# Performance work log

Measured on AMD Instinct MI355X. Metric: run time of the kernel, lower is better.

## Reference

```python
import jax, jax.numpy as jnp
import numpy as np
from jax import lax

FX, FY = 518.857, 519.469   # NYU-v2 depth intrinsics (cx/cy unused by forward)
B, H, W = 8, 479, 639       # TRAIN_CROP_SIZE = [W, H]; H+1, W+1 divisible by 4
P = 8                       # even PATCH_SIZE -> box-filter output is [H+1, W+1]
EPS = 1e-6


def _coords():
    # u_u0 = x - W/2, v_v0 = y - H/2, broadcast over [B,1,H,W]
    u = jnp.arange(W, dtype=jnp.float32)[None, None, None, :] - W / 2.0
    v = jnp.arange(H, dtype=jnp.float32)[None, None, :, None] - H / 2.0
    return u, v


def _surface_normal(xyz):
    # xyz: [H, W, 3] -> normals [H, W, 3]
    x, y, z = xyz[..., 0], xyz[..., 1], xyz[..., 2]
    # 9 box-filtered moments in a single depthwise conv (the original does 9 conv2d calls)
    mom = jnp.stack([x * x, x * y, x * z, y * y, y * z, z * z, x, y, z], 0)[None]  # [1,9,H,W]
    kern = jnp.ones((9, 1, P, P), xyz.dtype)
    s = lax.conv_general_dilated(mom, kern, (1, 1), [(P // 2, P // 2)] * 2,
                                 feature_group_count=9)[0]  # [9, H+1, W+1]
    xx, xy, xz, yy, yz, zz, xs, ys, zs = s
    ATA = jnp.stack([xx, xy, xz, xy, yy, yz, xz, yz, zz], -1)  # [H+1, W+1, 9]
    Hp, Wp = ATA.shape[0], ATA.shape[1]
    ATA = ATA.reshape(Hp, Wp, 3, 3) + EPS * jnp.eye(3, dtype=xyz.dtype)
    AT1 = jnp.stack([xs, ys, zs], -1)[..., None]  # [H+1, W+1, 3, 1]
    # original loops over 4x4 sub-patches with overlap=0 -> equivalent full-grid solve
    n = jnp.linalg.solve(ATA, AT1)                # [H+1, W+1, 3, 1]
    n = n / jnp.sqrt(jnp.sum(n * n, axis=2, keepdims=True))
    n = n[:-1, :-1, :, 0]                         # [H, W, 3]
    # orient toward camera: flip where dot(n, xyz) > 0
    flip = jnp.sum(n * xyz, axis=2, keepdims=True) > 0
    return jnp.where(flip, -n, n)


def _fit_normals(depth):
    # depth: [B,1,H,W] -> surface normals [B,3,H,W], zeroed where depth <= 0
    u, v = _coords()
    x = u * depth / FX
    y = v * depth / FY
    xyz = jnp.concatenate([x, y, depth], 1).transpose(0, 2, 3, 1)  # [B,H,W,3]
    sn = jax.vmap(_surface_normal)(xyz).transpose(0, 3, 1, 2)      # [B,3,H,W]
    return jnp.where(depth > 0, sn, 0.0)


def setup_inputs() -> dict:
    key = jax.random.key(0)
    k1, k2 = jax.random.split(key)
    prediction = jax.random.uniform(k1, (B, 1, H, W), jnp.float32)
    gt = jax.random.uniform(k2, (B, 1, H, W), jnp.float32)
    return {"prediction": prediction, "gt": gt}


def reference(prediction, gt):
    return jnp.mean(jnp.abs(_fit_normals(prediction) - _fit_normals(gt)))
```

## Files before the change

### kernel.cpp

```cpp
#include <hip/hip_runtime.h>

#define HH 479
#define WW 639
#define BATCH 8
#define NBLK (20 * 60 * 8)


__device__ __forceinline__ void solve_normal(
    float xx, float xy, float xz, float yy, float yz, float zz,
    float xs, float ys, float zs,
    float a_c, float b_c, float d0,
    float* nx, float* ny, float* nz)
{
    const float EPSV = 1e-6f;
    const float inv64 = 1.0f / 64.0f;
    float hx = xs * inv64, hy = ys * inv64, hz = zs * inv64;
    float cxx = fmaf(-hx, xs, xx) + EPSV;
    float cxy = fmaf(-hx, ys, xy);
    float cxz = fmaf(-hx, zs, xz);
    float cyy = fmaf(-hy, ys, yy) + EPSV;
    float cyz = fmaf(-hy, zs, yz);
    float czz = fmaf(-hz, zs, zz) + EPSV;
    float c00 = fmaf(cyy, czz, -cyz * cyz);
    float c01 = fmaf(cxz, cyz, -cxy * czz);
    float c02 = fmaf(cxy, cyz, -cxz * cyy);
    float c11 = fmaf(cxx, czz, -cxz * cxz);
    float c12 = fmaf(cxy, cxz, -cxx * cyz);
    float c22 = fmaf(cxx, cyy, -cxy * cxy);
    float m0 = fmaf(c00, xs, fmaf(c01, ys, c02 * zs));
    float m1 = fmaf(c01, xs, fmaf(c11, ys, c12 * zs));
    float m2 = fmaf(c02, xs, fmaf(c12, ys, c22 * zs));
    float g  = fmaf(m0, a_c, fmaf(m1, b_c, m2));
    float inv = rsqrtf(fmaf(m0, m0, fmaf(m1, m1, m2 * m2)));
    if (g > 0.0f) inv = -inv;
    if (!(d0 > 0.0f)) inv = 0.0f;
    *nx = m0 * inv; *ny = m1 * inv; *nz = m2 * inv;
}

__global__ __launch_bounds__(128, 7)
void ppal_main(const float* __restrict__ pred, const float* __restrict__ gt,
               double* __restrict__ acc)
{
    const int tx = threadIdx.x;
    const int ty = threadIdx.y;
    const int tid = ty * 16 + tx;
    const int j0 = blockIdx.x * 32;
    const int i0 = blockIdx.y * 8;
    const int b  = blockIdx.z;

    const float invFX = 1.0f / 518.857f;
    const float invFY = 1.0f / 519.469f;

    __shared__ float sd[2][15 * 41];
    __shared__ float4 cs4[312];
    __shared__ float  csTb[312];
    __shared__ float  wsum[2];

    const float* src0 = pred + (size_t)b * (HH * WW);
    const float* src1 = gt   + (size_t)b * (HH * WW);
    for (int idx = tid; idx < 15 * 41; idx += 128) {
        int lr = idx / 41, lc = idx - lr * 41;
        int r = i0 - 4 + lr, c = j0 - 4 + lc;
        bool ok = (lc < 39) && (r >= 0) && (r < HH) && (c >= 0) && (c < WW);
        int off = r * WW + c;
        sd[0][idx] = ok ? src0[off] : 0.0f;
        sd[1][idx] = ok ? src1[off] : 0.0f;
    }

    float aw[9];
#pragma unroll
    for (int m = 0; m < 9; ++m)
        aw[m] = ((float)(j0 + 2 * tx + m - 4) - 319.5f) * invFX;
    const float bc = ((float)(i0 + ty) - 239.5f) * invFY;
    const int ebase = ty * 39 + 2 * tx;

    float n0A[3], n1A[3];
    float contrib = 0.0f;

    __syncthreads();

#pragma unroll
    for (int k = 0; k < 2; ++k) {
        if (tid < 78) {
            int g = tid / 39;
            int c = tid - 39 * g;
            int rb = 4 * g;
            const float* col = &sd[k][c];
            float bv = ((float)(i0 + rb - 4) - 239.5f) * invFY;
            float S1 = 0.f, Sb = 0.f, Sbb = 0.f, T1 = 0.f, Tb = 0.f;
#pragma unroll
            for (int r = 0; r < 8; ++r) {
                float d  = col[(rb + r) * 41];
                float bvr = fmaf((float)r, invFY, bv);
                float bd = bvr * d;
                T1 += d;  Tb += bd;
                S1  = fmaf(d,  d,  S1);
                Sb  = fmaf(bd, d,  Sb);
                Sbb = fmaf(bd, bd, Sbb);
            }
            int e = rb * 39 + c;
            cs4[e]  = make_float4(S1, Sb, Sbb, T1);
            csTb[e] = Tb;
#pragma unroll
            for (int s = 1; s < 4; ++s) {
                float d0 = col[(rb + s - 1) * 41];
                float d1 = col[(rb + s + 7) * 41];
                float b0 = fmaf((float)(s - 1), invFY, bv);
                float b1 = fmaf((float)(s + 7), invFY, bv);
                float bd0 = b0 * d0, bd1 = b1 * d1;
                T1 += d1 - d0;
                Tb += bd1 - bd0;
                S1  += fmaf(d1,  d1,  -d0  * d0);
                Sb  += fmaf(bd1, d1,  -bd0 * d0);
                Sbb += fmaf(bd1, bd1, -bd0 * bd0);
                e += 39;
                cs4[e]  = make_float4(S1, Sb, Sbb, T1);
                csTb[e] = Tb;
            }
        }
        __syncthreads();

        {
            float Sxx = 0.f, Sxy = 0.f, Sxz = 0.f, Syy = 0.f, Syz = 0.f;
            float Szz = 0.f, Sxs = 0.f, Sys = 0.f, Szs = 0.f;
#pragma unroll
            for (int m = 1; m < 8; ++m) {
                int e = ebase + m;
                float4 r = cs4[e];
                float  tb = csTb[e];
                Szz += r.x;  Syz += r.y;  Syy += r.z;
                Szs += r.w;  Sys += tb;
                Sxz = fmaf(aw[m],         r.x, Sxz);
                Sxy = fmaf(aw[m],         r.y, Sxy);
                Sxs = fmaf(aw[m],         r.w, Sxs);
                Sxx = fmaf(aw[m] * aw[m], r.x, Sxx);
            }

            float nn[2][3];
#pragma unroll
            for (int p = 0; p < 2; ++p) {
                int m = (p == 0) ? 0 : 8;
                int e = ebase + m;
                float4 r = cs4[e];
                float  tb = csTb[e];
                float xx = fmaf(aw[m] * aw[m], r.x, Sxx);
                float xy = fmaf(aw[m], r.y, Sxy);
                float xz = fmaf(aw[m], r.x, Sxz);
                float yy = Syy + r.z;
                float yz = Syz + r.y;
                float zz = Szz + r.x;
                float xs = fmaf(aw[m], r.w, Sxs);
                float ys = Sys + tb;
                float zs = Szs + r.w;
                float d0 = sd[k][(ty + 4) * 41 + (2 * tx + p + 4)];
                solve_normal(xx, xy, xz, yy, yz, zz, xs, ys, zs,
                             aw[4 + p], bc, d0, &nn[p][0], &nn[p][1], &nn[p][2]);
            }
            if (k == 0) {
                n0A[0] = nn[0][0]; n0A[1] = nn[0][1]; n0A[2] = nn[0][2];
                n1A[0] = nn[1][0]; n1A[1] = nn[1][1]; n1A[2] = nn[1][2];
                __syncthreads();
            } else {
                const int i = i0 + ty;
                const bool valid0 = (i < HH);
                const bool valid1 = (i < HH) && (j0 + 2 * tx + 1 < WW);
                float c0 = fabsf(n0A[0] - nn[0][0]) + fabsf(n0A[1] - nn[0][1])
                         + fabsf(n0A[2] - nn[0][2]);
                float c1 = fabsf(n1A[0] - nn[1][0]) + fabsf(n1A[1] - nn[1][1])
                         + fabsf(n1A[2] - nn[1][2]);
                contrib = (valid0 ? c0 : 0.0f) + (valid1 ? c1 : 0.0f);
            }
        }
    }

    float v = contrib;
#pragma unroll
    for (int off = 32; off > 0; off >>= 1) v += __shfl_down(v, off, 64);
    int wid = tid >> 6, lane = tid & 63;
    if (lane == 0) wsum[wid] = v;
    __syncthreads();
    if (tid == 0) {
        double bs = (double)wsum[0] + (double)wsum[1];
        int slot = blockIdx.x + 20 * blockIdx.y + 1200 * blockIdx.z;
        acc[slot] = bs;
    }
}

__global__ void ppal_finalize(const double* __restrict__ acc, float* __restrict__ out)
{
    int tid = threadIdx.x;
    double v = 0.0;
    for (int s = tid; s < NBLK; s += 256) v += acc[s];
#pragma unroll
    for (int off = 32; off > 0; off >>= 1) v += __shfl_down(v, off, 64);
    __shared__ double wsum[4];
    int wid = tid >> 6, lane = tid & 63;
    if (lane == 0) wsum[wid] = v;
    __syncthreads();
    if (tid == 0)
        out[0] = (float)((wsum[0] + wsum[1] + wsum[2] + wsum[3])
                         * (1.0 / 7345944.0));
}

extern "C" void kernel_launch(void* const* d_in, const int* in_sizes, int n_in,
                              void* d_out, int out_size, void* d_ws, size_t ws_size,
                              hipStream_t stream)
{
    const float* pred = (const float*)d_in[0];
    const float* gt   = (const float*)d_in[1];
    float* out  = (float*)d_out;
    double* acc = (double*)d_ws;

    dim3 grid(20, 60, BATCH);
    dim3 block(16, 8);
    ppal_main<<<grid, block, 0, stream>>>(pred, gt, acc);
    ppal_finalize<<<1, 256, 0, stream>>>(acc, out);
}
```

Before: 101.7 us.

## Replace shared-memory box filter with per-wavefront sliding window and lane-permute sums

```diff
diff --git a/kernel.cpp b/kernel.cpp
--- a/kernel.cpp
+++ b/kernel.cpp
@@ -3,8 +3,19 @@
 #define HH 479
 #define WW 639
 #define BATCH 8
-#define NBLK (20 * 60 * 8)
-
+#define CT 12
+#define RB 30
+#define NBLK (CT * RB * BATCH)
+
+
+__device__ __forceinline__ float box8(float x, int a1, int a2, int a4)
+{
+    float t = x + __int_as_float(
+        __builtin_amdgcn_ds_bpermute(a1, __float_as_int(x)));
+    t += __int_as_float(__builtin_amdgcn_ds_bpermute(a2, __float_as_int(t)));
+    t += __int_as_float(__builtin_amdgcn_ds_bpermute(a4, __float_as_int(t)));
+    return t;
+}
 
 __device__ __forceinline__ void solve_normal(
     float xx, float xy, float xz, float yy, float yz, float zz,
@@ -37,152 +48,134 @@
     *nx = m0 * inv; *ny = m1 * inv; *nz = m2 * inv;
 }
 
-__global__ __launch_bounds__(128, 7)
+__global__ __launch_bounds__(64, 4)
 void ppal_main(const float* __restrict__ pred, const float* __restrict__ gt,
                double* __restrict__ acc)
 {
-    const int tx = threadIdx.x;
-    const int ty = threadIdx.y;
-    const int tid = ty * 16 + tx;
-    const int j0 = blockIdx.x * 32;
-    const int i0 = blockIdx.y * 8;
+    const int lane = threadIdx.x;
+    const int j0 = blockIdx.x * 56;
+    const int r0 = blockIdx.y * 16;
     const int b  = blockIdx.z;
 
     const float invFX = 1.0f / 518.857f;
     const float invFY = 1.0f / 519.469f;
 
-    __shared__ float sd[2][15 * 41];
-    __shared__ float4 cs4[312];
-    __shared__ float  csTb[312];
-    __shared__ float  wsum[2];
-
-    const float* src0 = pred + (size_t)b * (HH * WW);
-    const float* src1 = gt   + (size_t)b * (HH * WW);
-    for (int idx = tid; idx < 15 * 41; idx += 128) {
-        int lr = idx / 41, lc = idx - lr * 41;
-        int r = i0 - 4 + lr, c = j0 - 4 + lc;
-        bool ok = (lc < 39) && (r >= 0) && (r < HH) && (c >= 0) && (c < WW);
-        int off = r * WW + c;
-        sd[0][idx] = ok ? src0[off] : 0.0f;
-        sd[1][idx] = ok ? src1[off] : 0.0f;
+    const float* __restrict__ pA = pred + (size_t)b * (HH * WW);
+    const float* __restrict__ pB = gt   + (size_t)b * (HH * WW);
+
+    const int c = j0 - 4 + lane;
+    const int j = j0 + lane;
+    const bool col_ok = (c >= 0) && (c < WW);
+    const bool pix_ok = (lane < 56) && (j < WW);
+    const float a  = ((float)c - 319.5f) * invFX;
+    const float a2 = a * a;
+    const float ap = ((float)j - 319.5f) * invFX;
+    const int ba1 = ((lane + 1) & 63) << 2;
+    const int ba2 = ((lane + 2) & 63) << 2;
+    const int ba4 = ((lane + 4) & 63) << 2;
+
+    float S1A = 0.f, SbA = 0.f, SbbA = 0.f, T1A = 0.f, TbA = 0.f;
+    float S1B = 0.f, SbB = 0.f, SbbB = 0.f, T1B = 0.f, TbB = 0.f;
+
+    int off = (r0 - 4) * WW + c;
+#pragma unroll
+    for (int w = 0; w < 8; ++w) {
+        int r = r0 - 4 + w;
+        bool ok = col_ok && (r >= 0);
+        int o = ok ? off : 0;
+        float dA = pA[o]; dA = ok ? dA : 0.f;
+        float dB = pB[o]; dB = ok ? dB : 0.f;
+        float bv = ((float)r - 239.5f) * invFY;
+        float bdA = bv * dA, bdB = bv * dB;
+        T1A += dA;  TbA += bdA;
+        S1A = fmaf(dA,  dA,  S1A);
+        SbA = fmaf(bdA, dA,  SbA);
+        SbbA = fmaf(bdA, bdA, SbbA);
+        T1B += dB;  TbB += bdB;
+        S1B = fmaf(dB,  dB,  S1B);
+        SbB = fmaf(bdB, dB,  SbB);
+        SbbB = fmaf(bdB, bdB, SbbB);
+        off += WW;
     }
 
-    float aw[9];
-#pragma unroll
-    for (int m = 0; m < 9; ++m)
-        aw[m] = ((float)(j0 + 2 * tx + m - 4) - 319.5f) * invFX;
-    const float bc = ((float)(i0 + ty) - 239.5f) * invFY;
-    const int ebase = ty * 39 + 2 * tx;
-
-    float n0A[3], n1A[3];
-    float contrib = 0.0f;
-
-    __syncthreads();
-
-#pragma unroll
-    for (int k = 0; k < 2; ++k) {
-        if (tid < 78) {
-            int g = tid / 39;
-            int c = tid - 39 * g;
-            int rb = 4 * g;
-            const float* col = &sd[k][c];
-            float bv = ((float)(i0 + rb - 4) - 239.5f) * invFY;
-            float S1 = 0.f, Sb = 0.f, Sbb = 0.f, T1 = 0.f, Tb = 0.f;
-#pragma unroll
-            for (int r = 0; r < 8; ++r) {
-                float d  = col[(rb + r) * 41];
-                float bvr = fmaf((float)r, invFY, bv);
-                float bd = bvr * d;
-                T1 += d;  Tb += bd;
-                S1  = fmaf(d,  d,  S1);
-                Sb  = fmaf(bd, d,  Sb);
-                Sbb = fmaf(bd, bd, Sbb);
-            }
-            int e = rb * 39 + c;
-            cs4[e]  = make_float4(S1, Sb, Sbb, T1);
-            csTb[e] = Tb;
-#pragma unroll
-            for (int s = 1; s < 4; ++s) {
-                float d0 = col[(rb + s - 1) * 41];
-                float d1 = col[(rb + s + 7) * 41];
-                float b0 = fmaf((float)(s - 1), invFY, bv);
-                float b1 = fmaf((float)(s + 7), invFY, bv);
-                float bd0 = b0 * d0, bd1 = b1 * d1;
-                T1 += d1 - d0;
-                Tb += bd1 - bd0;
-                S1  += fmaf(d1,  d1,  -d0  * d0);
-                Sb  += fmaf(bd1, d1,  -bd0 * d0);
-                Sbb += fmaf(bd1, bd1, -bd0 * bd0);
-                e += 39;
-                cs4[e]  = make_float4(S1, Sb, Sbb, T1);
-                csTb[e] = Tb;
-            }
+    float contrib = 0.f;
+    int off_new = (r0 + 4) * WW + c;
+    int off_old = (r0 - 4) * WW + c;
+    int off_ctr = r0 * WW + j;
+
+    for (int s = 0; s < 16; ++s) {
+        const int i = r0 + s;
+        const bool row_ok = (i < HH);
+
+        {
+            const bool okc = row_ok && pix_ok;
+            int o = okc ? off_ctr : 0;
+            float d0A = pA[o]; d0A = okc ? d0A : 0.f;
+            float d0B = pB[o]; d0B = okc ? d0B : 0.f;
+            float bc = ((float)i - 239.5f) * invFY;
+
+            float hS1  = box8(S1A,      ba1, ba2, ba4);
+            float hSb  = box8(SbA,      ba1, ba2, ba4);
+            float hSbb = box8(SbbA,     ba1, ba2, ba4);
+            float hT1  = box8(T1A,      ba1, ba2, ba4);
+            float hTb  = box8(TbA,      ba1, ba2, ba4);
+            float haS1 = box8(a * S1A,  ba1, ba2, ba4);
+            float haSb = box8(a * SbA,  ba1, ba2, ba4);
+            float haT1 = box8(a * T1A,  ba1, ba2, ba4);
+            float ha2S1= box8(a2 * S1A, ba1, ba2, ba4);
+            float nA[3];
+            solve_normal(ha2S1, haSb, haS1, hSbb, hSb, hS1, haT1, hTb, hT1,
+                         ap, bc, d0A, &nA[0], &nA[1], &nA[2]);
+
+            float gS1  = box8(S1B,      ba1, ba2, ba4);
+            float gSb  = box8(SbB,      ba1, ba2, ba4);
+            float gSbb = box8(SbbB,     ba1, ba2, ba4);
+            float gT1  = box8(T1B,      ba1, ba2, ba4);
+            float gTb  = box8(TbB,      ba1, ba2, ba4);
+            float gaS1 = box8(a * S1B,  ba1, ba2, ba4);
+            float gaSb = box8(a * SbB,  ba1, ba2, ba4);
+            float gaT1 = box8(a * T1B,  ba1, ba2, ba4);
+            float ga2S1= box8(a2 * S1B, ba1, ba2, ba4);
+            float nB[3];
+            solve_normal(ga2S1, gaSb, gaS1, gSbb, gSb, gS1, gaT1, gTb, gT1,
+                         ap, bc, d0B, &nB[0], &nB[1], &nB[2]);
+
+            float cp = fabsf(nA[0] - nB[0]) + fabsf(nA[1] - nB[1])
+                     + fabsf(nA[2] - nB[2]);
+            contrib += okc ? cp : 0.f;
         }
-        __syncthreads();
 
         {
-            float Sxx = 0.f, Sxy = 0.f, Sxz = 0.f, Syy = 0.f, Syz = 0.f;
-            float Szz = 0.f, Sxs = 0.f, Sys = 0.f, Szs = 0.f;
-#pragma unroll
-            for (int m = 1; m < 8; ++m) {
-                int e = ebase + m;
-                float4 r = cs4[e];
-                float  tb = csTb[e];
-                Szz += r.x;  Syz += r.y;  Syy += r.z;
-                Szs += r.w;  Sys += tb;
-                Sxz = fmaf(aw[m],         r.x, Sxz);
-                Sxy = fmaf(aw[m],         r.y, Sxy);
-                Sxs = fmaf(aw[m],         r.w, Sxs);
-                Sxx = fmaf(aw[m] * aw[m], r.x, Sxx);
-            }
-
-            float nn[2][3];
-#pragma unroll
-            for (int p = 0; p < 2; ++p) {
-                int m = (p == 0) ? 0 : 8;
-                int e = ebase + m;
-                float4 r = cs4[e];
-                float  tb = csTb[e];
-                float xx = fmaf(aw[m] * aw[m], r.x, Sxx);
-                float xy = fmaf(aw[m], r.y, Sxy);
-                float xz = fmaf(aw[m], r.x, Sxz);
-                float yy = Syy + r.z;
-                float yz = Syz + r.y;
-                float zz = Szz + r.x;
-                float xs = fmaf(aw[m], r.w, Sxs);
-                float ys = Sys + tb;
-                float zs = Szs + r.w;
-                float d0 = sd[k][(ty + 4) * 41 + (2 * tx + p + 4)];
-                solve_normal(xx, xy, xz, yy, yz, zz, xs, ys, zs,
-                             aw[4 + p], bc, d0, &nn[p][0], &nn[p][1], &nn[p][2]);
-            }
-            if (k == 0) {
-                n0A[0] = nn[0][0]; n0A[1] = nn[0][1]; n0A[2] = nn[0][2];
-                n1A[0] = nn[1][0]; n1A[1] = nn[1][1]; n1A[2] = nn[1][2];
-                __syncthreads();
-            } else {
-                const int i = i0 + ty;
-                const bool valid0 = (i < HH);
-                const bool valid1 = (i < HH) && (j0 + 2 * tx + 1 < WW);
-                float c0 = fabsf(n0A[0] - nn[0][0]) + fabsf(n0A[1] - nn[0][1])
-                         + fabsf(n0A[2] - nn[0][2]);
-                float c1 = fabsf(n1A[0] - nn[1][0]) + fabsf(n1A[1] - nn[1][1])
-                         + fabsf(n1A[2] - nn[1][2]);
-                contrib = (valid0 ? c0 : 0.0f) + (valid1 ? c1 : 0.0f);
-            }
+            const bool okn = col_ok && (i + 4 < HH);
+            const bool oko = col_ok && (i - 4 >= 0);
+            int on = okn ? off_new : 0;
+            int oo = oko ? off_old : 0;
+            float dnA = pA[on]; dnA = okn ? dnA : 0.f;
+            float dnB = pB[on]; dnB = okn ? dnB : 0.f;
+            float doA = pA[oo]; doA = oko ? doA : 0.f;
+            float doB = pB[oo]; doB = oko ? doB : 0.f;
+            float bn = ((float)(i + 4) - 239.5f) * invFY;
+            float bo = ((float)(i - 4) - 239.5f) * invFY;
+            float bdnA = bn * dnA, bdoA = bo * doA;
+            float bdnB = bn * dnB, bdoB = bo * doB;
+            T1A += dnA - doA;   TbA += bdnA - bdoA;
+            S1A += fmaf(dnA,  dnA,  -doA  * doA);
+            SbA += fmaf(bdnA, dnA,  -bdoA * doA);
+            SbbA += fmaf(bdnA, bdnA, -bdoA * bdoA);
+            T1B += dnB - doB;   TbB += bdnB - bdoB;
+            S1B += fmaf(dnB,  dnB,  -doB  * doB);
+            SbB += fmaf(bdnB, dnB,  -bdoB * doB);
+            SbbB += fmaf(bdnB, bdnB, -bdoB * bdoB);
+            off_new += WW; off_old += WW; off_ctr += WW;
         }
     }
 
     float v = contrib;
 #pragma unroll
-    for (int off = 32; off > 0; off >>= 1) v += __shfl_down(v, off, 64);
-    int wid = tid >> 6, lane = tid & 63;
-    if (lane == 0) wsum[wid] = v;
-    __syncthreads();
-    if (tid == 0) {
-        double bs = (double)wsum[0] + (double)wsum[1];
-        int slot = blockIdx.x + 20 * blockIdx.y + 1200 * blockIdx.z;
-        acc[slot] = bs;
+    for (int o = 32; o > 0; o >>= 1) v += __shfl_down(v, o, 64);
+    if (lane == 0) {
+        int slot = blockIdx.x + CT * blockIdx.y + (CT * RB) * blockIdx.z;
+        acc[slot] = (double)v;
     }
 }
 
@@ -211,8 +204,8 @@
     float* out  = (float*)d_out;
     double* acc = (double*)d_ws;
 
-    dim3 grid(20, 60, BATCH);
-    dim3 block(16, 8);
+    dim3 grid(CT, RB, BATCH);
+    dim3 block(64);
     ppal_main<<<grid, block, 0, stream>>>(pred, gt, acc);
     ppal_finalize<<<1, 256, 0, stream>>>(acc, out);
 }
```

After: 108.6 us. 1.07x slower.
